# Performance work log

Measured on AMD Instinct MI355X. Metric: run time of the kernel, lower is better.

The kernel has to match this reference:

```python
import jax, jax.numpy as jnp
import numpy as np

N = 100000   # nodes
E = 1600000  # edges (before self-loops)
G = 128      # graphs in batch
IN = 128     # in_channels
H = 64       # GCN hidden dim
OUT = 7      # out_channels
N_STACK = 9  # 64->64 GCN layers after the first


def setup_inputs() -> dict:
    key = jax.random.key(0)
    ks = jax.random.split(key, 10)
    s = 0.1
    x = jax.random.normal(ks[0], (N, IN), dtype=jnp.float32)
    edge_index = jax.random.randint(ks[1], (2, E), 0, N, dtype=jnp.int32)
    batch = jnp.sort(jax.random.randint(ks[2], (N,), 0, G, dtype=jnp.int32))
    W0 = jax.random.normal(ks[3], (IN, H), dtype=jnp.float32) * s
    b0 = jnp.zeros((H,), dtype=jnp.float32)
    Ws = jax.random.normal(ks[4], (N_STACK, H, H), dtype=jnp.float32) * s
    bs = jnp.zeros((N_STACK, H), dtype=jnp.float32)
    Wlin = jax.random.normal(ks[5], (H, OUT), dtype=jnp.float32) * s
    blin = jnp.zeros((OUT,), dtype=jnp.float32)
    return {"x": x, "edge_index": edge_index, "batch": batch,
            "W0": W0, "b0": b0, "Ws": Ws, "bs": bs,
            "Wlin": Wlin, "blin": blin}


def reference(x, edge_index, batch, W0, b0, Ws, bs, Wlin, blin):
    # GCNConv with add_self_loops=True, normalize=True (PyG defaults):
    # out = D^{-1/2} (A + I) D^{-1/2} (X W) + b
    loop = jnp.arange(N, dtype=edge_index.dtype)
    src = jnp.concatenate([edge_index[0], loop])   # [E+N]
    dst = jnp.concatenate([edge_index[1], loop])   # [E+N]
    ones = jnp.ones_like(dst, dtype=x.dtype)
    deg = jax.ops.segment_sum(ones, dst, num_segments=N)       # in-degree incl. self-loop
    dinv = jnp.where(deg > 0, jax.lax.rsqrt(deg), 0.0)
    norm = dinv[src] * dinv[dst]                                # [E+N]

    def gcn(h, W, b):
        m = h @ W                                               # [N,H] linear first
        agg = jax.ops.segment_sum(norm[:, None] * m[src], dst, num_segments=N)
        return agg + b

    h = jax.nn.relu(gcn(x, W0, b0))
    # nn.Dropout / EvalDropout are identity in the deterministic reference

    def step(h, wb):
        W, b = wb
        return jax.nn.relu(gcn(h, W, b)), None

    h, _ = jax.lax.scan(step, h, (Ws, bs))                      # 9 stacked GCN layers

    # global_mean_pool over graph ids
    counts = jax.ops.segment_sum(jnp.ones((N,), dtype=h.dtype), batch, num_segments=G)
    pooled = jax.ops.segment_sum(h, batch, num_segments=G) / jnp.clip(counts, 1.0)[:, None]
    return pooled @ Wlin + blin                                 # [G, OUT]
```

## Files before the change

kernel.cpp:

```cpp
#include <hip/hip_runtime.h>
#include <hip/hip_fp16.h>

#define NNODES 100000
#define NEDGES 1600000
#define NGRAPH 128
#define CIN 128
#define CH 64
#define COUT 7
#define NSTACK 9

#define NB 391
#define CHUNK 2048
#define NC 782

typedef __attribute__((ext_vector_type(8))) short bf16x8;
typedef __attribute__((ext_vector_type(4))) float f32x4;

__device__ __forceinline__ unsigned short f2bf(float f) {
    unsigned u = __float_as_uint(f);
    return (unsigned short)((u + 0x7FFFu + ((u >> 16) & 1u)) >> 16);
}

__global__ __launch_bounds__(256) void hist_gemm_kernel(const int* __restrict__ dst,
                                                        int* __restrict__ hist, int E,
                                                        const float* __restrict__ h,
                                                        const float* __restrict__ W,
                                                        __half* __restrict__ m, int N,
                                                        int histBlocks) {
    __shared__ alignas(16) char smem[32768 + 2048];
    if (blockIdx.x < (unsigned)histBlocks) {
        int* lh = (int*)smem;
        for (int i = threadIdx.x; i < NB; i += 256) lh[i] = 0;
        __syncthreads();
        int e0 = blockIdx.x * CHUNK;
        int e1 = min(e0 + CHUNK, E);
        for (int e = e0 + threadIdx.x; e < e1; e += 256)
            atomicAdd(&lh[dst[e] >> 8], 1);
        __syncthreads();
        for (int i = threadIdx.x; i < NB; i += 256) hist[i * NC + (int)blockIdx.x] = lh[i];
        return;
    }
    int gb = blockIdx.x - histBlocks;
    unsigned short* wf_hi = (unsigned short*)smem;
    unsigned short* wf_lo = wf_hi + 16 * 64 * 8;
    int t = threadIdx.x;

    {
        int c = t >> 4;
        int kstep = c >> 2, ncol = c & 3;
        int l0 = (t & 15) * 4;
        for (int dl = 0; dl < 4; ++dl) {
            int l = l0 + dl;
            int kbase = kstep * 32 + (l >> 4) * 8;
            int n = ncol * 16 + (l & 15);
            for (int i = 0; i < 8; ++i) {
                float wv = W[(size_t)(kbase + i) * 64 + n];
                unsigned short hb = f2bf(wv);
                float hf = __uint_as_float(((unsigned)hb) << 16);
                wf_hi[((size_t)c * 64 + l) * 8 + i] = hb;
                wf_lo[((size_t)c * 64 + l) * 8 + i] = f2bf(wv - hf);
            }
        }
    }
    __syncthreads();

    int wave = t >> 6, lane = t & 63;
    long row0 = (long)gb * 64 + wave * 16;
    if (row0 >= N) return;

    long arow = row0 + (lane & 15);
    const float4* xr = (const float4*)(h + (size_t)arow * 128);
    int kg = lane >> 4;

    f32x4 zero = {0.0f, 0.0f, 0.0f, 0.0f};
    f32x4 acc[4];
    acc[0] = zero; acc[1] = zero; acc[2] = zero; acc[3] = zero;

#pragma unroll
    for (int s = 0; s < 4; ++s) {
        float4 p = xr[s * 8 + kg * 2];
        float4 q = xr[s * 8 + kg * 2 + 1];
        float xv[8] = {p.x, p.y, p.z, p.w, q.x, q.y, q.z, q.w};
        bf16x8 a_hi, a_lo;
#pragma unroll
        for (int i = 0; i < 8; ++i) {
            unsigned short hb = f2bf(xv[i]);
            a_hi[i] = (short)hb;
            a_lo[i] = (short)f2bf(xv[i] - __uint_as_float(((unsigned)hb) << 16));
        }
#pragma unroll
        for (int nc = 0; nc < 4; ++nc) {
            int c = s * 4 + nc;
            bf16x8 b_hi = *(const bf16x8*)(wf_hi + ((size_t)c * 64 + lane) * 8);
            bf16x8 b_lo = *(const bf16x8*)(wf_lo + ((size_t)c * 64 + lane) * 8);
            acc[nc] = __builtin_amdgcn_mfma_f32_16x16x32_bf16(a_hi, b_hi, acc[nc], 0, 0, 0);
            acc[nc] = __builtin_amdgcn_mfma_f32_16x16x32_bf16(a_hi, b_lo, acc[nc], 0, 0, 0);
            acc[nc] = __builtin_amdgcn_mfma_f32_16x16x32_bf16(a_lo, b_hi, acc[nc], 0, 0, 0);
        }
    }

    int drow = (lane >> 4) * 4;
    int dcol = lane & 15;
#pragma unroll
    for (int nc = 0; nc < 4; ++nc)
#pragma unroll
        for (int r = 0; r < 4; ++r)
            m[(size_t)(row0 + drow + r) * 64 + nc * 16 + dcol] = __float2half(acc[nc][r]);
}

__global__ void pack_wfrags_kernel(const float* __restrict__ Ws,
                                   unsigned short* __restrict__ wfh,
                                   unsigned short* __restrict__ wfl) {
    int b = blockIdx.x;
    int l = b >> 3, c = b & 7;
    int s = c >> 2, nc = c & 3;
    for (int v = threadIdx.x; v < 512; v += 256) {
        int L = v >> 3, i = v & 7;
        int k = s * 32 + (L >> 4) * 8 + i;
        int n = nc * 16 + (L & 15);
        float w = Ws[(size_t)l * 4096 + k * 64 + n];
        unsigned short hb = f2bf(w);
        float hf = __uint_as_float(((unsigned)hb) << 16);
        size_t idx = ((size_t)b * 64 + L) * 8 + i;
        wfh[idx] = hb;
        wfl[idx] = f2bf(w - hf);
    }
}

__global__ __launch_bounds__(256) void scan_chunks_kernel(int* __restrict__ hist,
                                                          int* __restrict__ btot) {
    int b = blockIdx.x;
    int t = threadIdx.x;
    int* row = hist + b * NC;
    int v[4];
    int base = 4 * t;
#pragma unroll
    for (int u = 0; u < 4; ++u) v[u] = (base + u < NC) ? row[base + u] : 0;
    int tsum = v[0] + v[1] + v[2] + v[3];
    __shared__ int s[256];
    s[t] = tsum;
    __syncthreads();
    for (int d = 1; d < 256; d <<= 1) {
        int x = (t >= d) ? s[t - d] : 0;
        __syncthreads();
        s[t] += x;
        __syncthreads();
    }
    int run = s[t] - tsum;
    if (t == 255) btot[b] = s[255];
#pragma unroll
    for (int u = 0; u < 4; ++u) {
        if (base + u < NC) row[base + u] = run;
        run += v[u];
    }
}

__global__ void scan_buckets_kernel(const int* __restrict__ tot, int* __restrict__ out) {
    __shared__ int s[512];
    int t = threadIdx.x;
    int v = (t < NB) ? tot[t] : 0;
    s[t] = v;
    __syncthreads();
    for (int d = 1; d < 512; d <<= 1) {
        int x = (t >= d) ? s[t - d] : 0;
        __syncthreads();
        s[t] += x;
        __syncthreads();
    }
    if (t < NB) out[t] = s[t] - v;
    if (t == NB - 1) out[NB] = s[t];
}

__global__ __launch_bounds__(256) void scatter_kernel(const int* __restrict__ src,
                                                      const int* __restrict__ dst,
                                                      const int* __restrict__ hist,
                                                      const int* __restrict__ bbase,
                                                      int* __restrict__ src_b,
                                                      int* __restrict__ dst_b, int E) {
    __shared__ int offs[NB];
    for (int b = threadIdx.x; b < NB; b += 256)
        offs[b] = hist[b * NC + (int)blockIdx.x] + bbase[b];
    __syncthreads();
    int e0 = blockIdx.x * CHUNK;
    int e1 = min(e0 + CHUNK, E);
    for (int e = e0 + threadIdx.x; e < e1; e += 256) {
        int d = dst[e], s = src[e];
        int pos = atomicAdd(&offs[d >> 8], 1);
        src_b[pos] = s;
        dst_b[pos] = d;
    }
}

__global__ __launch_bounds__(256) void bucket_prep_kernel(const int* __restrict__ dst_b,
                                                          const int* __restrict__ bbase,
                                                          const int* __restrict__ btot,
                                                          int* __restrict__ rowptr,
                                                          int* __restrict__ pbt,
                                                          float* __restrict__ dinv,
                                                          const int* __restrict__ batch,
                                                          int* __restrict__ gcnt, int N) {
    if ((int)blockIdx.x == NB) {
        int g = threadIdx.x;
        if (g >= NGRAPH) return;
        auto lb = [&](int v) {
            int lo = 0, hi = N;
            while (lo < hi) {
                int mid = (lo + hi) >> 1;
                if (batch[mid] < v) lo = mid + 1; else hi = mid;
            }
            return lo;
        };
        gcnt[g] = lb(g + 1) - lb(g);
        return;
    }
    __shared__ int c256[256];
    __shared__ int s[256];
    int t = threadIdx.x;
    c256[t] = 0;
    __syncthreads();
    int lo = bbase[blockIdx.x], n = btot[blockIdx.x];
    for (int e = lo + t; e < lo + n; e += 256) atomicAdd(&c256[dst_b[e] & 255], 1);
    __syncthreads();
    int cnt = c256[t];
    int pcnt = (cnt + 7) & ~7;
    s[t] = pcnt;
    __syncthreads();
    for (int d = 1; d < 256; d <<= 1) {
        int x = (t >= d) ? s[t - d] : 0;
        __syncthreads();
        s[t] += x;
        __syncthreads();
    }
    int node = blockIdx.x * 256 + t;
    if (node < N) {
        rowptr[node] = s[t] - pcnt;
        dinv[node] = 1.0f / sqrtf((float)(cnt + 1));
    }
    if (t == 255) pbt[blockIdx.x] = s[255];
}

__global__ void rowptr_fix_kernel(int* __restrict__ rowptr, const int* __restrict__ pbbase,
                                  int N) {
    int i = blockIdx.x * 256 + threadIdx.x;
    if (i < N) rowptr[i] += pbbase[i >> 8];
    if (i == 0) rowptr[N] = pbbase[NB];
}

__global__ __launch_bounds__(256) void bucket_fill_kernel(const int* __restrict__ src_b,
                                                          const int* __restrict__ dst_b,
                                                          const int* __restrict__ bbase,
                                                          const int* __restrict__ btot,
                                                          const int* __restrict__ rowptr,
                                                          int* __restrict__ col, int N) {
    __shared__ int f256[256];
    __shared__ int rp[256];
    int t = threadIdx.x;
    f256[t] = 0;
    int node = blockIdx.x * 256 + t;
    rp[t] = (node < N) ? rowptr[node] : 0;
    __syncthreads();
    int lo = bbase[blockIdx.x], n = btot[blockIdx.x];
    for (int e = lo + t; e < lo + n; e += 256) {
        int d = dst_b[e], sv = src_b[e];
        int li = d & 255;
        int slot = atomicAdd(&f256[li], 1);
        col[rp[li] + slot] = sv;
    }
    __syncthreads();
    if (node < N) {
        int c = f256[t];
        int pc = (c + 7) & ~7;
        int base = rp[t];
        for (int p = c; p < pc; ++p) col[base + p] = N;
    }
}

__global__ __launch_bounds__(256) void scale_m_kernel(__half* __restrict__ m,
                                                      __half* __restrict__ other,
                                                      const float* __restrict__ dinv, int N) {
    if (blockIdx.x == 0 && threadIdx.x < 64) {
        m[(size_t)N * 64 + threadIdx.x] = __float2half(0.0f);
        other[(size_t)N * 64 + threadIdx.x] = __float2half(0.0f);
    }
    int tot = N * 32;
    __half2* m2 = (__half2*)m;
    for (int idx = blockIdx.x * 256 + threadIdx.x; idx < tot; idx += gridDim.x * 256) {
        float d = dinv[idx >> 5];
        float2 f = __half22float2(m2[idx]);
        f.x *= d;
        f.y *= d;
        m2[idx] = __float22half2_rn(f);
    }
}

__device__ __forceinline__ void pair_gather(const __half* __restrict__ h,
                                            const int* __restrict__ col,
                                            int r0, int mid, int r1, int lane,
                                            float& aA, float& aB) {
    int n = r1 - r0;
    int e = 0;
    for (; e + 16 <= n; e += 16) {
        int base = r0 + e;
        int c[16];
        float v[16];
#pragma unroll
        for (int u = 0; u < 16; ++u) c[u] = col[base + u];
#pragma unroll
        for (int u = 0; u < 16; ++u) v[u] = __half2float(h[(size_t)c[u] * 64 + lane]);
        float s0 = ((v[0] + v[1]) + (v[2] + v[3])) + ((v[4] + v[5]) + (v[6] + v[7]));
        float s1 = ((v[8] + v[9]) + (v[10] + v[11])) + ((v[12] + v[13]) + (v[14] + v[15]));
        bool b0 = (base < mid);
        bool b1 = (base + 8 < mid);
        aA += b0 ? s0 : 0.0f;
        aB += b0 ? 0.0f : s0;
        aA += b1 ? s1 : 0.0f;
        aB += b1 ? 0.0f : s1;
    }
    if (e + 8 <= n) {
        int base = r0 + e;
        int c[8];
        float v[8];
#pragma unroll
        for (int u = 0; u < 8; ++u) c[u] = col[base + u];
#pragma unroll
        for (int u = 0; u < 8; ++u) v[u] = __half2float(h[(size_t)c[u] * 64 + lane]);
        float s0 = ((v[0] + v[1]) + (v[2] + v[3])) + ((v[4] + v[5]) + (v[6] + v[7]));
        bool b0 = (base < mid);
        aA += b0 ? s0 : 0.0f;
        aB += b0 ? 0.0f : s0;
    }
}

__global__ __launch_bounds__(256) void agg0_kernel(const __half* __restrict__ m,
                                                   const int* __restrict__ rowptr,
                                                   const int* __restrict__ col,
                                                   const float* __restrict__ dinv,
                                                   const float* __restrict__ bias,
                                                   __half* __restrict__ hout, int N) {
    int wid = __builtin_amdgcn_readfirstlane((blockIdx.x * 256 + threadIdx.x) >> 6);
    int lane = threadIdx.x & 63;
    int nodeA = wid * 2;
    int nodeB = nodeA + 1;
    if (nodeA >= N) return;
    int r0 = rowptr[nodeA];
    int mid = rowptr[nodeB];
    int r1 = rowptr[nodeB + 1];
    float diA = dinv[nodeA], diB = dinv[nodeB];
    float aA = __half2float(m[(size_t)nodeA * 64 + lane]);
    float aB = __half2float(m[(size_t)nodeB * 64 + lane]);
    pair_gather(m, col, r0, mid, r1, lane, aA, aB);
    float bv = bias[lane];
    float hA = fmaxf(diA * aA + bv, 0.0f);
    float hB = fmaxf(diB * aB + bv, 0.0f);
    hout[(size_t)nodeA * 64 + lane] = __float2half(diA * hA);
    hout[(size_t)nodeB * 64 + lane] = __float2half(diB * hB);
}

__global__ __launch_bounds__(256) void fused_kernel(const __half* __restrict__ h,
                                                    const int* __restrict__ rowptr,
                                                    const int* __restrict__ col,
                                                    const float* __restrict__ dinv,
                                                    const unsigned short* __restrict__ wfh,
                                                    const unsigned short* __restrict__ wfl,
                                                    const float* __restrict__ bias,
                                                    __half* __restrict__ hout, int N,
                                                    int scaleOut) {
    __shared__ float gLds[16][68];

    int wave = __builtin_amdgcn_readfirstlane((int)(threadIdx.x >> 6));
    int lane = threadIdx.x & 63;
    int node0 = blockIdx.x * 8;
    int nodeA = node0 + wave * 2;
    int nodeB = nodeA + 1;

    int r0 = rowptr[nodeA];
    int mid = rowptr[nodeB];
    int r1 = rowptr[nodeB + 1];
    float diA = dinv[nodeA], diB = dinv[nodeB];
    float aA = __half2float(h[(size_t)nodeA * 64 + lane]);
    float aB = __half2float(h[(size_t)nodeB * 64 + lane]);
    pair_gather(h, col, r0, mid, r1, lane, aA, aB);
    gLds[wave * 2][lane] = diA * aA;
    gLds[wave * 2 + 1][lane] = diB * aB;

    __syncthreads();

    int arow = lane & 15;
    int kg = lane >> 4;
    f32x4 acc = {0.0f, 0.0f, 0.0f, 0.0f};
#pragma unroll
    for (int s = 0; s < 2; ++s) {
        const float* ap = &gLds[arow][s * 32 + kg * 8];
        float xv[8];
#pragma unroll
        for (int i = 0; i < 8; ++i) xv[i] = ap[i];
        union { bf16x8 v; unsigned u[4]; } ahi, alo;
#pragma unroll
        for (int p = 0; p < 4; ++p) {
            unsigned u0 = __float_as_uint(xv[2 * p]);
            unsigned u1 = __float_as_uint(xv[2 * p + 1]);
            ahi.u[p] = __builtin_amdgcn_perm(u1, u0, 0x07060302);
            float l0 = xv[2 * p] - __uint_as_float(u0 & 0xFFFF0000u);
            float l1 = xv[2 * p + 1] - __uint_as_float(u1 & 0xFFFF0000u);
            unsigned r;
            asm("v_cvt_pk_bf16_f32 %0, %1, %2" : "=v"(r) : "v"(l0), "v"(l1));
            alo.u[p] = r;
        }
        const bf16x8 b_hi = *(const bf16x8*)(wfh + ((size_t)(s * 4 + wave) * 64 + lane) * 8);
        const bf16x8 b_lo = *(const bf16x8*)(wfl + ((size_t)(s * 4 + wave) * 64 + lane) * 8);
        acc = __builtin_amdgcn_mfma_f32_16x16x32_bf16(ahi.v, b_hi, acc, 0, 0, 0);
        acc = __builtin_amdgcn_mfma_f32_16x16x32_bf16(ahi.v, b_lo, acc, 0, 0, 0);
        acc = __builtin_amdgcn_mfma_f32_16x16x32_bf16(alo.v, b_hi, acc, 0, 0, 0);
    }

    int dcol = wave * 16 + (lane & 15);
    int rbase = (lane >> 4) * 4;
    if (rbase < 8) {
        float bv = bias[dcol];
#pragma unroll
        for (int r = 0; r < 4; ++r) {
            int nd = node0 + rbase + r;
            float v = fmaxf(acc[r] + bv, 0.0f);
            if (scaleOut) v *= dinv[nd];
            hout[(size_t)nd * 64 + dcol] = __float2half(v);
        }
    }
}

__global__ __launch_bounds__(256) void pool_kernel(const __half* __restrict__ h,
                                                   const int* __restrict__ batch,
                                                   float* __restrict__ gpool, int N) {
    const int NPW = 32;
    int wid = (blockIdx.x * 256 + threadIdx.x) >> 6;
    int lane = threadIdx.x & 63;
    int i0 = wid * NPW;
    if (i0 >= N) return;
    int i1 = min(i0 + NPW, N);
    int curg = batch[i0];
    float acc = 0.0f;
    for (int i = i0; i < i1; ++i) {
        int g = batch[i];
        if (g != curg) {
            atomicAdd(&gpool[curg * 64 + lane], acc);
            acc = 0.0f;
            curg = g;
        }
        acc += __half2float(h[(size_t)i * 64 + lane]);
    }
    atomicAdd(&gpool[curg * 64 + lane], acc);
}

__global__ void final_kernel(const float* __restrict__ gpool, const int* __restrict__ gcnt,
                             const float* __restrict__ Wlin, const float* __restrict__ blin,
                             float* __restrict__ out) {
    int t = threadIdx.x;
    if (t >= NGRAPH * COUT) return;
    int g = t / COUT, o = t - g * COUT;
    float c = (float)gcnt[g];
    if (c < 1.0f) c = 1.0f;
    float s = 0.0f;
    for (int k = 0; k < 64; ++k) s += gpool[g * 64 + k] * Wlin[k * COUT + o];
    out[t] = s / c + blin[o];
}

extern "C" void kernel_launch(void* const* d_in, const int* in_sizes, int n_in,
                              void* d_out, int out_size, void* d_ws, size_t ws_size,
                              hipStream_t stream) {
    const float* x    = (const float*)d_in[0];
    const int*   ei   = (const int*)d_in[1];
    const int*   batch= (const int*)d_in[2];
    const float* W0   = (const float*)d_in[3];
    const float* b0   = (const float*)d_in[4];
    const float* Ws   = (const float*)d_in[5];
    const float* bs   = (const float*)d_in[6];
    const float* Wlin = (const float*)d_in[7];
    const float* blin = (const float*)d_in[8];
    float* out = (float*)d_out;

    const int N = NNODES, E = NEDGES;
    const int* srcp = ei;
    const int* dstp = ei + E;

    char* w = (char*)d_ws;
    float* gpool  = (float*)w; w += (size_t)NGRAPH * 64 * 4;
    size_t zero_bytes = (size_t)(w - (char*)d_ws);
    int*   gcnt   = (int*)w;   w += (size_t)NGRAPH * 4;
    float* dinv   = (float*)w; w += (size_t)N * 4;
    int*   rowptr = (int*)w;   w += (size_t)(N + 1) * 4;
    int*   hist   = (int*)w;   w += (size_t)NB * NC * 4;
    int*   btot   = (int*)w;   w += (size_t)NB * 4;
    int*   bbase  = (int*)w;   w += (size_t)(NB + 1) * 4;
    int*   pbt    = (int*)w;   w += (size_t)NB * 4;
    int*   pbbase = (int*)w;   w += (size_t)(NB + 1) * 4;
    int*   src_b  = (int*)w;   w += (size_t)E * 4;
    int*   dst_b  = (int*)w;   w += (size_t)E * 4;
    int*   col    = (int*)w;   w += ((size_t)E + 8 * N) * 4;
    unsigned short* wfh = (unsigned short*)w; w += (size_t)NSTACK * 4096 * 2;
    unsigned short* wfl = (unsigned short*)w; w += (size_t)NSTACK * 4096 * 2;
    __half* bufA  = (__half*)w; w += (size_t)(N + 1) * 64 * 2;
    __half* bufB  = (__half*)w; w += (size_t)(N + 1) * 64 * 2;

    hipMemsetAsync(d_ws, 0, zero_bytes, stream);

    int nblocks = (N + 255) / 256;
    int gemmblocks = (N + 63) / 64;

    pack_wfrags_kernel<<<NSTACK * 8, 256, 0, stream>>>(Ws, wfh, wfl);
    hist_gemm_kernel<<<NC + gemmblocks, 256, 0, stream>>>(
        dstp, hist, E, x, W0, bufB, N, NC);
    scan_chunks_kernel<<<NB, 256, 0, stream>>>(hist, btot);
    scan_buckets_kernel<<<1, 512, 0, stream>>>(btot, bbase);
    scatter_kernel<<<NC, 256, 0, stream>>>(srcp, dstp, hist, bbase, src_b, dst_b, E);
    bucket_prep_kernel<<<NB + 1, 256, 0, stream>>>(dst_b, bbase, btot, rowptr, pbt, dinv,
                                                   batch, gcnt, N);
    scan_buckets_kernel<<<1, 512, 0, stream>>>(pbt, pbbase);
    rowptr_fix_kernel<<<nblocks, 256, 0, stream>>>(rowptr, pbbase, N);
    bucket_fill_kernel<<<NB, 256, 0, stream>>>(src_b, dst_b, bbase, btot, rowptr, col, N);
    scale_m_kernel<<<2048, 256, 0, stream>>>(bufB, bufA, dinv, N);

    int pairblocks = (N / 2 + 3) / 4;
    int fusedblocks = N / 8;

    agg0_kernel<<<pairblocks, 256, 0, stream>>>(bufB, rowptr, col, dinv, b0, bufA, N);

    __half* hin = bufA;
    __half* hout = bufB;
    for (int l = 0; l < NSTACK; ++l) {
        int scaleOut = (l < NSTACK - 1) ? 1 : 0;
        fused_kernel<<<fusedblocks, 256, 0, stream>>>(hin, rowptr, col, dinv,
                                                      wfh + (size_t)l * 4096,
                                                      wfl + (size_t)l * 4096,
                                                      bs + (size_t)l * 64, hout, N,
                                                      scaleOut);
        __half* t = hin; hin = hout; hout = t;
    }

    int pwaves = (N + 31) / 32;
    int pblocks = (pwaves + 3) / 4;
    pool_kernel<<<pblocks, 256, 0, stream>>>(hin, batch, gpool, N);
    final_kernel<<<1, 896, 0, stream>>>(gpool, gcnt, Wlin, blin, out);
}
```

Baseline: 626.5 us.

## Split scatter into 8 bucket classes and pack edges as int2

The scatter kernel now launches eight blocks per edge chunk, and each block handles only the destination buckets whose index mod 8 matches its class. This raises parallelism and spreads the shared-memory atomics. Source and destination are stored together as one int2 array instead of two int arrays, so the prep and fill kernels read one 8-byte element per edge. The cost is that each chunk's dst array is read eight times, and each class writes fewer, sparser positions.

```diff
diff --git a/kernel.cpp b/kernel.cpp
--- a/kernel.cpp
+++ b/kernel.cpp
@@ -175,23 +175,26 @@
                                                       const int* __restrict__ dst,
                                                       const int* __restrict__ hist,
                                                       const int* __restrict__ bbase,
-                                                      int* __restrict__ src_b,
-                                                      int* __restrict__ dst_b, int E) {
+                                                      int2* __restrict__ edge_b, int E) {
     __shared__ int offs[NB];
+    int ck = blockIdx.x >> 3;
+    int cls = blockIdx.x & 7;
     for (int b = threadIdx.x; b < NB; b += 256)
-        offs[b] = hist[b * NC + (int)blockIdx.x] + bbase[b];
-    __syncthreads();
-    int e0 = blockIdx.x * CHUNK;
+        offs[b] = hist[b * NC + ck] + bbase[b];
+    __syncthreads();
+    int e0 = ck * CHUNK;
     int e1 = min(e0 + CHUNK, E);
     for (int e = e0 + threadIdx.x; e < e1; e += 256) {
-        int d = dst[e], s = src[e];
-        int pos = atomicAdd(&offs[d >> 8], 1);
-        src_b[pos] = s;
-        dst_b[pos] = d;
-    }
-}
-
-__global__ __launch_bounds__(256) void bucket_prep_kernel(const int* __restrict__ dst_b,
+        int d = dst[e];
+        if (((d >> 8) & 7) == cls) {
+            int s = src[e];
+            int pos = atomicAdd(&offs[d >> 8], 1);
+            edge_b[pos] = make_int2(s, d);
+        }
+    }
+}
+
+__global__ __launch_bounds__(256) void bucket_prep_kernel(const int2* __restrict__ edge_b,
                                                           const int* __restrict__ bbase,
                                                           const int* __restrict__ btot,
                                                           int* __restrict__ rowptr,
@@ -219,7 +222,7 @@
     c256[t] = 0;
     __syncthreads();
     int lo = bbase[blockIdx.x], n = btot[blockIdx.x];
-    for (int e = lo + t; e < lo + n; e += 256) atomicAdd(&c256[dst_b[e] & 255], 1);
+    for (int e = lo + t; e < lo + n; e += 256) atomicAdd(&c256[edge_b[e].y & 255], 1);
     __syncthreads();
     int cnt = c256[t];
     int pcnt = (cnt + 7) & ~7;
@@ -246,8 +249,7 @@
     if (i == 0) rowptr[N] = pbbase[NB];
 }
 
-__global__ __launch_bounds__(256) void bucket_fill_kernel(const int* __restrict__ src_b,
-                                                          const int* __restrict__ dst_b,
+__global__ __launch_bounds__(256) void bucket_fill_kernel(const int2* __restrict__ edge_b,
                                                           const int* __restrict__ bbase,
                                                           const int* __restrict__ btot,
                                                           const int* __restrict__ rowptr,
@@ -261,10 +263,10 @@
     __syncthreads();
     int lo = bbase[blockIdx.x], n = btot[blockIdx.x];
     for (int e = lo + t; e < lo + n; e += 256) {
-        int d = dst_b[e], sv = src_b[e];
-        int li = d & 255;
+        int2 ed = edge_b[e];
+        int li = ed.y & 255;
         int slot = atomicAdd(&f256[li], 1);
-        col[rp[li] + slot] = sv;
+        col[rp[li] + slot] = ed.x;
     }
     __syncthreads();
     if (node < N) {
@@ -492,8 +494,7 @@
     int*   bbase  = (int*)w;   w += (size_t)(NB + 1) * 4;
     int*   pbt    = (int*)w;   w += (size_t)NB * 4;
     int*   pbbase = (int*)w;   w += (size_t)(NB + 1) * 4;
-    int*   src_b  = (int*)w;   w += (size_t)E * 4;
-    int*   dst_b  = (int*)w;   w += (size_t)E * 4;
+    int2*  edge_b = (int2*)w;  w += (size_t)E * 8;
     int*   col    = (int*)w;   w += ((size_t)E + 8 * N) * 4;
     unsigned short* wfh = (unsigned short*)w; w += (size_t)NSTACK * 4096 * 2;
     unsigned short* wfl = (unsigned short*)w; w += (size_t)NSTACK * 4096 * 2;
@@ -510,12 +511,12 @@
         dstp, hist, E, x, W0, bufB, N, NC);
     scan_chunks_kernel<<<NB, 256, 0, stream>>>(hist, btot);
     scan_buckets_kernel<<<1, 512, 0, stream>>>(btot, bbase);
-    scatter_kernel<<<NC, 256, 0, stream>>>(srcp, dstp, hist, bbase, src_b, dst_b, E);
-    bucket_prep_kernel<<<NB + 1, 256, 0, stream>>>(dst_b, bbase, btot, rowptr, pbt, dinv,
+    scatter_kernel<<<NC * 8, 256, 0, stream>>>(srcp, dstp, hist, bbase, edge_b, E);
+    bucket_prep_kernel<<<NB + 1, 256, 0, stream>>>(edge_b, bbase, btot, rowptr, pbt, dinv,
                                                    batch, gcnt, N);
     scan_buckets_kernel<<<1, 512, 0, stream>>>(pbt, pbbase);
     rowptr_fix_kernel<<<nblocks, 256, 0, stream>>>(rowptr, pbbase, N);
-    bucket_fill_kernel<<<NB, 256, 0, stream>>>(src_b, dst_b, bbase, btot, rowptr, col, N);
+    bucket_fill_kernel<<<NB, 256, 0, stream>>>(edge_b, bbase, btot, rowptr, col, N);
     scale_m_kernel<<<2048, 256, 0, stream>>>(bufB, bufA, dinv, N);
 
     int pairblocks = (N / 2 + 3) / 4;
```

Result: no change. 623.0 us (median of 2 runs) (-0.6%).
